# Kernel optimization log

Measured on AMD Instinct MI355X. Metric: run time of the kernel, lower is better.

Reference implementation:

```python
import jax, jax.numpy as jnp
import numpy as np

B, L, D_MODEL, H = 2, 2048, 256, 8
D_HEAD = D_MODEL // H


def setup_inputs() -> dict:
    key = jax.random.key(0)
    ks = jax.random.split(key, 12)
    queries = jax.random.normal(ks[0], (B, L, D_MODEL), dtype=jnp.float32)
    keys_ = jax.random.normal(ks[1], (B, L, D_MODEL), dtype=jnp.float32)
    values = jax.random.normal(ks[2], (B, L, D_MODEL), dtype=jnp.float32)
    attention_mask = jax.random.randint(ks[3], (B, L, L), 0, 2, dtype=jnp.int32)
    adjacency_matrix = jax.random.uniform(ks[4], (B, L, L), dtype=jnp.float32)
    dist = jax.random.normal(ks[5], (B, L, L), dtype=jnp.float32)
    # row-subtracted distance matrix (each row minus its row max), per docstring
    distance_matrix = dist - jnp.max(dist, axis=-1, keepdims=True)
    s = 1.0 / np.sqrt(D_MODEL)
    Wq = jax.random.normal(ks[6], (D_MODEL, D_MODEL), dtype=jnp.float32) * s
    Wk = jax.random.normal(ks[7], (D_MODEL, D_MODEL), dtype=jnp.float32) * s
    Wv = jax.random.normal(ks[8], (D_MODEL, D_MODEL), dtype=jnp.float32) * s
    Wo = jax.random.normal(ks[9], (D_MODEL, D_MODEL), dtype=jnp.float32) * s
    weight_A = jax.random.normal(ks[10], (1, H, 1, 1), dtype=jnp.float32)
    weight_D = jax.random.normal(ks[11], (1, H, 1, 1), dtype=jnp.float32)
    return {"queries": queries, "keys": keys_, "values": values,
            "attention_mask": attention_mask, "adjacency_matrix": adjacency_matrix,
            "distance_matrix": distance_matrix, "Wq": Wq, "Wk": Wk, "Wv": Wv,
            "Wo": Wo, "weight_A": weight_A, "weight_D": weight_D}


def reference(queries, keys, values, attention_mask, adjacency_matrix,
              distance_matrix, Wq, Wk, Wv, Wo, weight_A, weight_D):
    b, l = queries.shape[0], queries.shape[1]
    # projections (nn.Linear: x @ W.T), split into heads -> (b, h, l, d_head)
    def proj(x, W):
        return (x @ W.T).reshape(b, l, H, D_HEAD).transpose(0, 2, 1, 3)
    Q, K, V = proj(queries, Wq), proj(keys, Wk), proj(values, Wv)
    scale = jnp.float32(D_HEAD) ** 0.5
    # raw scores (b, h, lq, lk)
    score = jnp.einsum('bhqd,bhkd->bhqk', Q, K)
    # mask: 1 valid, 0 invalid; masked positions filled with 0.0
    M = attention_mask[:, None, :, :]  # (b,1,l,l)
    score = jnp.where(M == 1, score, 0.0)
    A = adjacency_matrix[:, None]   # (b,1,l,l)
    Ds = distance_matrix[:, None]   # (b,1,l,l)
    score = score + score * (A * weight_A) + score * (Ds * weight_D)
    attn = jax.nn.softmax(score / scale, axis=-1)
    out = jnp.einsum('bhqk,bhkd->bhqd', attn, V)
    out = out.transpose(0, 2, 1, 3).reshape(b, l, D_MODEL)
    return out @ Wo.T, attn
```

## Files before the change

### kernel.cpp

```cpp
#include <hip/hip_runtime.h>
#include <math.h>

#define BB 2
#define LL 2048
#define DMODEL 256
#define NH 8
#define DHEAD 32
#define LL2 (LL*LL)
#define NQ (BB*NH*LL*DHEAD)

constexpr float SCALE_INV = 0.17677669529663687f;

__global__ __launch_bounds__(256) void proj_kernel(
    const float* __restrict__ xq, const float* __restrict__ xk, const float* __restrict__ xv,
    const float* __restrict__ Wq, const float* __restrict__ Wk, const float* __restrict__ Wv,
    float* __restrict__ Qo, float* __restrict__ Ko, float* __restrict__ Vo,
    float* __restrict__ Q15, float* __restrict__ K15)
{
    const float* X; const float* W; float* O; float* dup;
    if (blockIdx.z == 0)      { X = xq; W = Wq; O = Qo; dup = Q15; }
    else if (blockIdx.z == 1) { X = xk; W = Wk; O = Ko; dup = K15; }
    else                      { X = xv; W = Wv; O = Vo; dup = nullptr; }

    __shared__ float Xs[64][33];
    __shared__ float Ws[64][33];

    const int t  = threadIdx.x;
    const int m0 = blockIdx.x * 64;
    const int n0 = blockIdx.y * 64;
    const int ty = t >> 4;
    const int tx = t & 15;

    float acc[4][4] = {};

    for (int k0 = 0; k0 < DMODEL; k0 += 32) {
#pragma unroll
        for (int r = 0; r < 2; ++r) {
            int f   = t + 256 * r;
            int row = f >> 3;
            int c   = (f & 7) << 2;
            float4 xv4 = *(const float4*)(X + (size_t)(m0 + row) * DMODEL + k0 + c);
            Xs[row][c+0] = xv4.x; Xs[row][c+1] = xv4.y; Xs[row][c+2] = xv4.z; Xs[row][c+3] = xv4.w;
            float4 wv4 = *(const float4*)(W + (size_t)(n0 + row) * DMODEL + k0 + c);
            Ws[row][c+0] = wv4.x; Ws[row][c+1] = wv4.y; Ws[row][c+2] = wv4.z; Ws[row][c+3] = wv4.w;
        }
        __syncthreads();
#pragma unroll
        for (int kk = 0; kk < 32; ++kk) {
            float a[4], bv[4];
#pragma unroll
            for (int i = 0; i < 4; ++i) a[i]  = Xs[ty*4+i][kk];
#pragma unroll
            for (int j = 0; j < 4; ++j) bv[j] = Ws[tx*4+j][kk];
#pragma unroll
            for (int i = 0; i < 4; ++i)
#pragma unroll
                for (int j = 0; j < 4; ++j)
                    acc[i][j] = fmaf(a[i], bv[j], acc[i][j]);
        }
        __syncthreads();
    }

#pragma unroll
    for (int i = 0; i < 4; ++i) {
        int row = m0 + ty*4 + i;
        int b   = row / LL;
        int l   = row % LL;
#pragma unroll
        for (int j = 0; j < 4; ++j) {
            int col = n0 + tx*4 + j;
            int h   = col >> 5;
            int d   = col & 31;
            O[(size_t)(((b*NH + h)*LL) + l) * DHEAD + d] = acc[i][j];
            if (dup && row >= LL && col >= 224) {
                dup[(size_t)(row - LL) * DHEAD + (col - 224)] = acc[i][j];
            }
        }
    }
}

__global__ __launch_bounds__(256, 3) void attn_main_kernel(
    const float* __restrict__ Q, const float* __restrict__ K, const float* __restrict__ V,
    const int* __restrict__ mask, const float* __restrict__ adj, const float* __restrict__ dist,
    const float* __restrict__ wA, const float* __restrict__ wD,
    float* __restrict__ attn, float* __restrict__ ctx,
    float* __restrict__ Mall, float* __restrict__ Sall,
    float* __restrict__ Mw, float* __restrict__ Sw)
{
    const int t    = threadIdx.x;
    const int bh   = blockIdx.y;
    const int b    = bh >> 3;
    const int h    = bh & 7;
    const int q0   = blockIdx.x * 32;
    const int kcol = t & 63;
    const int wid  = t >> 6;
    const int dcol = t & 31;
    const int grp  = t >> 5;

    __shared__ float Qs[32][36];
    __shared__ float Ks[64][36];
    __shared__ float Vs[64][36];
    __shared__ float As[32][68];

    const float wa = wA[h];
    const float wd = wD[h];

    {
        int row = t >> 3;
        int c   = (t & 7) << 2;
        float4 qv = *(const float4*)(Q + (size_t)(bh * LL + q0 + row) * DHEAD + c);
        Qs[row][c+0] = qv.x; Qs[row][c+1] = qv.y; Qs[row][c+2] = qv.z; Qs[row][c+3] = qv.w;
    }

    float m[8], s[8];
#pragma unroll
    for (int j = 0; j < 8; ++j) { m[j] = -INFINITY; s[j] = 0.0f; }
    float acc[4] = {0.f, 0.f, 0.f, 0.f};

    const size_t kv_base = (size_t)bh * LL * DHEAD;
    const size_t mrow    = (size_t)(b * LL + q0);

    float fm[8];
#pragma unroll
    for (int j = 0; j < 8; ++j) {
        size_t mi = (mrow + wid + 4*j) * LL + kcol;
        int   mk = mask[mi];
        float a  = adj[mi];
        float d  = dist[mi];
        fm[j] = (mk == 1) ? (1.0f + a*wa + d*wd) : 0.0f;
    }

    for (int kt = 0; kt < 32; ++kt) {
#pragma unroll
        for (int r = 0; r < 2; ++r) {
            int f   = t + 256 * r;
            int row = f >> 3;
            int c   = (f & 7) << 2;
            float4 kv = *(const float4*)(K + kv_base + (size_t)(kt*64 + row) * DHEAD + c);
            Ks[row][c+0]=kv.x; Ks[row][c+1]=kv.y; Ks[row][c+2]=kv.z; Ks[row][c+3]=kv.w;
            float4 vv = *(const float4*)(V + kv_base + (size_t)(kt*64 + row) * DHEAD + c);
            Vs[row][c+0]=vv.x; Vs[row][c+1]=vv.y; Vs[row][c+2]=vv.z; Vs[row][c+3]=vv.w;
        }
        __syncthreads();

        float4 kf[8];
        {
            const float4* kp = (const float4*)&Ks[kcol][0];
#pragma unroll
            for (int c = 0; c < 8; ++c) kf[c] = kp[c];
        }

        const int kg = kt*64 + kcol;
        float lv[8];
#pragma unroll
        for (int j = 0; j < 8; ++j) {
            int qq = wid + 4*j;
            float s0 = 0.f;
            const float4* qp = (const float4*)&Qs[qq][0];
#pragma unroll
            for (int c = 0; c < 8; ++c) {
                float4 q4 = qp[c];
                s0 += q4.x*kf[c].x + q4.y*kf[c].y + q4.z*kf[c].z + q4.w*kf[c].w;
            }
            lv[j] = s0 * fm[j] * SCALE_INV;
            if (bh != 15) attn[(size_t)(bh * LL + q0 + qq) * LL + kg] = lv[j];
        }

        float mloc[8];
#pragma unroll
        for (int j = 0; j < 8; ++j) mloc[j] = lv[j];
#pragma unroll
        for (int off = 1; off < 64; off <<= 1)
#pragma unroll
            for (int j = 0; j < 8; ++j)
                mloc[j] = fmaxf(mloc[j], __shfl_xor(mloc[j], off, 64));

#pragma unroll
        for (int j = 0; j < 8; ++j) {
            int qq = wid + 4*j;
            float mnew  = fmaxf(m[j], mloc[j]);
            float alpha = __expf(m[j] - mnew);
            float p     = __expf(lv[j] - mnew);
            s[j] = s[j]*alpha + p;
            m[j] = mnew;
            As[qq][kcol] = p;
            if (kcol == 0) As[qq][64] = alpha;
        }
        __syncthreads();

        if (kt + 1 < 32) {
            const int kgn = (kt+1)*64 + kcol;
#pragma unroll
            for (int j = 0; j < 8; ++j) {
                size_t mi = (mrow + wid + 4*j) * LL + kgn;
                int   mk = mask[mi];
                float a  = adj[mi];
                float d  = dist[mi];
                fm[j] = (mk == 1) ? (1.0f + a*wa + d*wd) : 0.0f;
            }
        }

        float sum[4] = {0.f, 0.f, 0.f, 0.f};
#pragma unroll
        for (int c = 0; c < 16; ++c) {
            int kl = c * 4;
            float v0 = Vs[kl+0][dcol];
            float v1 = Vs[kl+1][dcol];
            float v2 = Vs[kl+2][dcol];
            float v3 = Vs[kl+3][dcol];
#pragma unroll
            for (int jj = 0; jj < 4; ++jj) {
                float4 a4 = *(const float4*)&As[grp*4+jj][kl];
                sum[jj] += a4.x*v0 + a4.y*v1 + a4.z*v2 + a4.w*v3;
            }
        }
#pragma unroll
        for (int jj = 0; jj < 4; ++jj) {
            int r = grp*4 + jj;
            acc[jj] = acc[jj]*As[r][64] + sum[jj];
        }
        __syncthreads();
    }

#pragma unroll
    for (int j = 0; j < 8; ++j) {
        float ss = s[j];
#pragma unroll
        for (int off = 1; off < 64; off <<= 1)
            ss += __shfl_xor(ss, off, 64);
        float inv = 1.0f / ss;
        int qq = wid + 4*j;
        int qg = q0 + qq;
        if (kcol == 0) {
            As[qq][65] = inv;
            if (bh != 15) { Mall[bh*LL + qg] = m[j]; Sall[bh*LL + qg] = inv; }
            else          { Mw[qg] = m[j];           Sw[qg] = inv; }
        }
    }
    __syncthreads();

#pragma unroll
    for (int jj = 0; jj < 4; ++jj) {
        int r  = grp*4 + jj;
        int qg = q0 + r;
        ctx[(size_t)(bh * LL + qg) * DHEAD + dcol] = acc[jj] * As[r][65];
    }
}

__global__ __launch_bounds__(256) void rescale_kernel(
    float* __restrict__ attn, const float* __restrict__ Mall, const float* __restrict__ Sall)
{
    size_t tid = (size_t)blockIdx.x * 256 + threadIdx.x;
    size_t e4  = tid * 4;
    int bh  = (int)(e4 >> 22);
    int row = (int)((e4 >> 11) & (LL - 1));
    float Mv = Mall[bh*LL + row];
    float Sv = Sall[bh*LL + row];
    float4* p = (float4*)(attn + e4);
    float4 v = *p;
    v.x = __expf(v.x - Mv) * Sv;
    v.y = __expf(v.y - Mv) * Sv;
    v.z = __expf(v.z - Mv) * Sv;
    v.w = __expf(v.w - Mv) * Sv;
    *p = v;
}

__global__ __launch_bounds__(256) void out_gemm_kernel(
    const float* __restrict__ ctx, const float* __restrict__ Wo, float* __restrict__ Y)
{
    __shared__ float Xs[64][33];
    __shared__ float Ws[64][33];

    const int t  = threadIdx.x;
    const int m0 = blockIdx.x * 64;
    const int n0 = blockIdx.y * 64;
    const int ty = t >> 4;
    const int tx = t & 15;

    float acc[4][4] = {};

    for (int kt = 0; kt < 8; ++kt) {
#pragma unroll
        for (int r = 0; r < 2; ++r) {
            int f   = t + 256*r;
            int row = f >> 3;
            int c   = (f & 7) << 2;
            int grow = m0 + row;
            int b = grow / LL, l = grow % LL;
            float4 xv4 = *(const float4*)(ctx + (size_t)((b*NH + kt)*LL + l) * DHEAD + c);
            Xs[row][c+0]=xv4.x; Xs[row][c+1]=xv4.y; Xs[row][c+2]=xv4.z; Xs[row][c+3]=xv4.w;
            float4 wv4 = *(const float4*)(Wo + (size_t)(n0 + row) * DMODEL + kt*32 + c);
            Ws[row][c+0]=wv4.x; Ws[row][c+1]=wv4.y; Ws[row][c+2]=wv4.z; Ws[row][c+3]=wv4.w;
        }
        __syncthreads();
#pragma unroll
        for (int kk = 0; kk < 32; ++kk) {
            float a[4], bv[4];
#pragma unroll
            for (int i = 0; i < 4; ++i) a[i]  = Xs[ty*4+i][kk];
#pragma unroll
            for (int j = 0; j < 4; ++j) bv[j] = Ws[tx*4+j][kk];
#pragma unroll
            for (int i = 0; i < 4; ++i)
#pragma unroll
                for (int j = 0; j < 4; ++j)
                    acc[i][j] = fmaf(a[i], bv[j], acc[i][j]);
        }
        __syncthreads();
    }

#pragma unroll
    for (int i = 0; i < 4; ++i) {
        int row = m0 + ty*4 + i;
#pragma unroll
        for (int j = 0; j < 4; ++j) {
            int col = n0 + tx*4 + j;
            Y[(size_t)row * DMODEL + col] = acc[i][j];
        }
    }
}

__global__ __launch_bounds__(256) void attn15_kernel(
    const float* __restrict__ Q15, const float* __restrict__ K15,
    const int* __restrict__ mask, const float* __restrict__ adj, const float* __restrict__ dist,
    const float* __restrict__ wA, const float* __restrict__ wD,
    const float* __restrict__ Mw, const float* __restrict__ Sw,
    float* __restrict__ attn15)
{
    const int t    = threadIdx.x;
    const int q0   = blockIdx.x * 32;
    const int kt0  = blockIdx.y * 2;
    const int kcol = t & 63;
    const int wid  = t >> 6;

    __shared__ float Qs[32][36];
    __shared__ float Ks[128][36];

    const float wa = wA[7];
    const float wd = wD[7];

    {
        int row = t >> 3;
        int c   = (t & 7) << 2;
        float4 qv = *(const float4*)(Q15 + (size_t)(q0 + row) * DHEAD + c);
        Qs[row][c+0] = qv.x; Qs[row][c+1] = qv.y; Qs[row][c+2] = qv.z; Qs[row][c+3] = qv.w;
    }

    float Mr[8], Sr[8];
#pragma unroll
    for (int j = 0; j < 8; ++j) {
        int qg = q0 + wid + 4*j;
        Mr[j] = Mw[qg];
        Sr[j] = Sw[qg];
    }

    for (int kt = kt0; kt < kt0 + 2; ++kt) {
#pragma unroll
        for (int r = 0; r < 4; ++r) {
            int f   = t + 256 * r;
            int row = f >> 3;
            int c   = (f & 7) << 2;
            float4 kv = *(const float4*)(K15 + (size_t)(kt*128 + row) * DHEAD + c);
            Ks[row][c+0]=kv.x; Ks[row][c+1]=kv.y; Ks[row][c+2]=kv.z; Ks[row][c+3]=kv.w;
        }
        __syncthreads();

        float4 k0[8], k1[8];
        {
            const float4* p0 = (const float4*)&Ks[kcol][0];
            const float4* p1 = (const float4*)&Ks[kcol + 64][0];
#pragma unroll
            for (int c = 0; c < 8; ++c) { k0[c] = p0[c]; k1[c] = p1[c]; }
        }

        const int kg0 = kt*128 + kcol;
#pragma unroll
        for (int j = 0; j < 8; ++j) {
            int qq = wid + 4*j;
            float s0 = 0.f, s1 = 0.f;
            const float4* qp = (const float4*)&Qs[qq][0];
#pragma unroll
            for (int c = 0; c < 8; ++c) {
                float4 q4 = qp[c];
                s0 += q4.x*k0[c].x + q4.y*k0[c].y + q4.z*k0[c].z + q4.w*k0[c].w;
                s1 += q4.x*k1[c].x + q4.y*k1[c].y + q4.z*k1[c].z + q4.w*k1[c].w;
            }
            int qg = q0 + qq;
            size_t mi0 = (size_t)(LL + qg) * LL + kg0;
            size_t mi1 = mi0 + 64;
            float sm0 = (mask[mi0] == 1) ? s0 : 0.0f;
            float sm1 = (mask[mi1] == 1) ? s1 : 0.0f;
            float l0 = sm0 * (1.0f + adj[mi0]*wa + dist[mi0]*wd) * SCALE_INV;
            float l1 = sm1 * (1.0f + adj[mi1]*wa + dist[mi1]*wd) * SCALE_INV;
            size_t ai = (size_t)qg * LL + kg0;
            attn15[ai]      = __expf(l0 - Mr[j]) * Sr[j];
            attn15[ai + 64] = __expf(l1 - Mr[j]) * Sr[j];
        }
        __syncthreads();
    }
}

extern "C" void kernel_launch(void* const* d_in, const int* in_sizes, int n_in,
                              void* d_out, int out_size, void* d_ws, size_t ws_size,
                              hipStream_t stream)
{
    const float* q    = (const float*)d_in[0];
    const float* k    = (const float*)d_in[1];
    const float* v    = (const float*)d_in[2];
    const int*   mask = (const int*)d_in[3];
    const float* adj  = (const float*)d_in[4];
    const float* dist = (const float*)d_in[5];
    const float* Wq   = (const float*)d_in[6];
    const float* Wk   = (const float*)d_in[7];
    const float* Wv   = (const float*)d_in[8];
    const float* Wo   = (const float*)d_in[9];
    const float* wA   = (const float*)d_in[10];
    const float* wD   = (const float*)d_in[11];

    float* out  = (float*)d_out;
    float* attn = out + (size_t)BB*LL*DMODEL;

    float* tail = attn + (size_t)15 * LL2;
    float* Qw = tail;
    float* Kw = tail + (size_t)NQ;
    float* Vw = tail + (size_t)2 * NQ;
    float* Cw = tail + (size_t)3 * NQ;

    float* Mall = out;
    float* Sall = out + 32768;

    float* Q15 = (float*)d_ws;
    float* K15 = Q15 + (size_t)LL * DHEAD;
    float* Mw  = K15 + (size_t)LL * DHEAD;
    float* Sw  = Mw + LL;

    dim3 g1(64, 4, 3);
    proj_kernel<<<g1, 256, 0, stream>>>(q, k, v, Wq, Wk, Wv, Qw, Kw, Vw, Q15, K15);

    dim3 g2(LL/32, BB*NH);
    attn_main_kernel<<<g2, 256, 0, stream>>>(Qw, Kw, Vw, mask, adj, dist, wA, wD,
                                             attn, Cw, Mall, Sall, Mw, Sw);

    rescale_kernel<<<15 * LL2 / 4 / 256, 256, 0, stream>>>(attn, Mall, Sall);

    dim3 g3(64, 4);
    out_gemm_kernel<<<g3, 256, 0, stream>>>(Cw, Wo, out);

    dim3 g4(64, 8);
    attn15_kernel<<<g4, 256, 0, stream>>>(Q15, K15, mask, adj, dist, wA, wD, Mw, Sw,
                                          attn + (size_t)15 * LL2);
}
```

Baseline: 1.255 ms.

## Recompute attention logits in final pass instead of storing and rescaling them

The main attention kernel no longer writes unnormalized logits to the attention output. A new final kernel recomputes Q·K and the mask/adjacency/distance factor per tile, then writes normalized probabilities using the saved row max and inverse sum. This removes a full write-then-read-modify-write pass over the large attention tensor. In exchange it adds extra QK FLOPs and rereads of the mask and auxiliary matrices per head.

New measurement: 1.262 ms. About the same (+0.6%).

```diff
diff --git a/kernel.cpp b/kernel.cpp
--- a/kernel.cpp
+++ b/kernel.cpp
@@ -83,7 +83,7 @@
     const float* __restrict__ Q, const float* __restrict__ K, const float* __restrict__ V,
     const int* __restrict__ mask, const float* __restrict__ adj, const float* __restrict__ dist,
     const float* __restrict__ wA, const float* __restrict__ wD,
-    float* __restrict__ attn, float* __restrict__ ctx,
+    float* __restrict__ ctx,
     float* __restrict__ Mall, float* __restrict__ Sall,
     float* __restrict__ Mw, float* __restrict__ Sw)
 {
@@ -150,7 +150,6 @@
             for (int c = 0; c < 8; ++c) kf[c] = kp[c];
         }
 
-        const int kg = kt*64 + kcol;
         float lv[8];
 #pragma unroll
         for (int j = 0; j < 8; ++j) {
@@ -163,7 +162,6 @@
                 s0 += q4.x*kf[c].x + q4.y*kf[c].y + q4.z*kf[c].z + q4.w*kf[c].w;
             }
             lv[j] = s0 * fm[j] * SCALE_INV;
-            if (bh != 15) attn[(size_t)(bh * LL + q0 + qq) * LL + kg] = lv[j];
         }
 
         float mloc[8];
@@ -247,22 +245,90 @@
     }
 }
 
-__global__ __launch_bounds__(256) void rescale_kernel(
-    float* __restrict__ attn, const float* __restrict__ Mall, const float* __restrict__ Sall)
+__global__ __launch_bounds__(256) void attn_final_kernel(
+    const float* __restrict__ Q, const float* __restrict__ K,
+    const int* __restrict__ mask, const float* __restrict__ adj, const float* __restrict__ dist,
+    const float* __restrict__ wA, const float* __restrict__ wD,
+    const float* __restrict__ Mall, const float* __restrict__ Sall,
+    float* __restrict__ attn)
 {
-    size_t tid = (size_t)blockIdx.x * 256 + threadIdx.x;
-    size_t e4  = tid * 4;
-    int bh  = (int)(e4 >> 22);
-    int row = (int)((e4 >> 11) & (LL - 1));
-    float Mv = Mall[bh*LL + row];
-    float Sv = Sall[bh*LL + row];
-    float4* p = (float4*)(attn + e4);
-    float4 v = *p;
-    v.x = __expf(v.x - Mv) * Sv;
-    v.y = __expf(v.y - Mv) * Sv;
-    v.z = __expf(v.z - Mv) * Sv;
-    v.w = __expf(v.w - Mv) * Sv;
-    *p = v;
+    const int t    = threadIdx.x;
+    const int bh   = blockIdx.z;
+    const int b    = bh >> 3;
+    const int h    = bh & 7;
+    const int q0   = blockIdx.x * 32;
+    const int kt0  = blockIdx.y * 2;
+    const int kcol = t & 63;
+    const int wid  = t >> 6;
+
+    __shared__ float Qs[32][36];
+    __shared__ float Ks[128][36];
+
+    const float wa = wA[h];
+    const float wd = wD[h];
+
+    const size_t qk_base = (size_t)bh * LL * DHEAD;
+    float* aout = attn + (size_t)bh * LL2;
+
+    {
+        int row = t >> 3;
+        int c   = (t & 7) << 2;
+        float4 qv = *(const float4*)(Q + qk_base + (size_t)(q0 + row) * DHEAD + c);
+        Qs[row][c+0] = qv.x; Qs[row][c+1] = qv.y; Qs[row][c+2] = qv.z; Qs[row][c+3] = qv.w;
+    }
+
+    float Mr[8], Sr[8];
+#pragma unroll
+    for (int j = 0; j < 8; ++j) {
+        int qg = q0 + wid + 4*j;
+        Mr[j] = Mall[bh*LL + qg];
+        Sr[j] = Sall[bh*LL + qg];
+    }
+
+    for (int kt = kt0; kt < kt0 + 2; ++kt) {
+#pragma unroll
+        for (int r = 0; r < 4; ++r) {
+            int f   = t + 256 * r;
+            int row = f >> 3;
+            int c   = (f & 7) << 2;
+            float4 kv = *(const float4*)(K + qk_base + (size_t)(kt*128 + row) * DHEAD + c);
+            Ks[row][c+0]=kv.x; Ks[row][c+1]=kv.y; Ks[row][c+2]=kv.z; Ks[row][c+3]=kv.w;
+        }
+        __syncthreads();
+
+        float4 k0[8], k1[8];
+        {
+            const float4* p0 = (const float4*)&Ks[kcol][0];
+            const float4* p1 = (const float4*)&Ks[kcol + 64][0];
+#pragma unroll
+            for (int c = 0; c < 8; ++c) { k0[c] = p0[c]; k1[c] = p1[c]; }
+        }
+
+        const int kg0 = kt*128 + kcol;
+#pragma unroll
+        for (int j = 0; j < 8; ++j) {
+            int qq = wid + 4*j;
+            float s0 = 0.f, s1 = 0.f;
+            const float4* qp = (const float4*)&Qs[qq][0];
+#pragma unroll
+            for (int c = 0; c < 8; ++c) {
+                float4 q4 = qp[c];
+                s0 += q4.x*k0[c].x + q4.y*k0[c].y + q4.z*k0[c].z + q4.w*k0[c].w;
+                s1 += q4.x*k1[c].x + q4.y*k1[c].y + q4.z*k1[c].z + q4.w*k1[c].w;
+            }
+            int qg = q0 + qq;
+            size_t mi0 = (size_t)(b * LL + qg) * LL + kg0;
+            size_t mi1 = mi0 + 64;
+            float fm0 = (mask[mi0] == 1) ? (1.0f + adj[mi0]*wa + dist[mi0]*wd) : 0.0f;
+            float fm1 = (mask[mi1] == 1) ? (1.0f + adj[mi1]*wa + dist[mi1]*wd) : 0.0f;
+            float l0 = s0 * fm0 * SCALE_INV;
+            float l1 = s1 * fm1 * SCALE_INV;
+            size_t ai = (size_t)qg * LL + kg0;
+            aout[ai]      = __expf(l0 - Mr[j]) * Sr[j];
+            aout[ai + 64] = __expf(l1 - Mr[j]) * Sr[j];
+        }
+        __syncthreads();
+    }
 }
 
 __global__ __launch_bounds__(256) void out_gemm_kernel(
@@ -439,9 +505,11 @@
 
     dim3 g2(LL/32, BB*NH);
     attn_main_kernel<<<g2, 256, 0, stream>>>(Qw, Kw, Vw, mask, adj, dist, wA, wD,
-                                             attn, Cw, Mall, Sall, Mw, Sw);
-
-    rescale_kernel<<<15 * LL2 / 4 / 256, 256, 0, stream>>>(attn, Mall, Sall);
+                                             Cw, Mall, Sall, Mw, Sw);
+
+    dim3 gf(64, 8, 15);
+    attn_final_kernel<<<gf, 256, 0, stream>>>(Qw, Kw, mask, adj, dist, wA, wD,
+                                              Mall, Sall, attn);
 
     dim3 g3(64, 4);
     out_gemm_kernel<<<g3, 256, 0, stream>>>(Cw, Wo, out);
```
